# Optimization experiments

Measured on AMD Instinct MI355X. Metric: run time of the kernel, lower is better.

The kernel has to match this reference:

```python
import jax, jax.numpy as jnp
import numpy as np
from jax import lax

NB_ITER = 100
TOL = 1e-6
DN = ('NCHW', 'OIHW', 'NCHW')
PAD = ((1, 1), (1, 1))


def _P(x, kernel):
    # x: [B,H,W] -> [B,3,H,W], conv2d with kernel [3,1,3,3], padding=1
    return lax.conv_general_dilated(x[:, None], kernel, (1, 1), PAD, dimension_numbers=DN)


def _PT(x, kernel):
    # x: [B,3,H,W] -> [B,H,W]; conv_transpose2d(padding=1) == conv2d with
    # spatially-flipped kernel and in/out channels swapped.
    kt = jnp.flip(kernel, (2, 3)).transpose(1, 0, 2, 3)  # [1,3,3,3]
    return lax.conv_general_dilated(x, kt, (1, 1), PAD, dimension_numbers=DN)[:, 0]


def _cg(A, b):
    # Conjugate gradient; original: while i <= 100 and crit >= tol (101 iters max).
    x = b
    r = b - A(x)
    p = r
    crit = jnp.sum(r * r)

    def body(carry, _):
        x, r, p, crit = carry
        active = crit >= TOL
        Ap = A(p)
        denom = jnp.sum(p * Ap)
        alpha = crit / jnp.where(active, denom, 1.0)
        x_n = x + alpha * p
        r_n = r - alpha * Ap
        crit_n = jnp.sum(r_n * r_n)
        beta = crit_n / jnp.where(active, crit, 1.0)
        p_n = r_n + beta * p
        x = jnp.where(active, x_n, x)
        r = jnp.where(active, r_n, r)
        p = jnp.where(active, p_n, p)
        crit = jnp.where(active, crit_n, crit)
        return (x, r, p, crit), None

    (x, _, _, _), _ = lax.scan(body, (x, r, p, crit), None, length=NB_ITER + 1)
    return x


def setup_inputs() -> dict:
    key = jax.random.key(0)
    ks = jax.random.split(key, 6)
    B, C, H, W = 4, 3, 256, 256
    return {
        'mask': jax.random.uniform(ks[0], (B, C, H, W), dtype=jnp.float32),
        'y': jax.random.uniform(ks[1], (B, H, W), dtype=jnp.float32),
        'z': jax.random.normal(ks[2], (B, C, H, W), dtype=jnp.float32),
        'beta': jax.random.normal(ks[3], (B, C, H, W), dtype=jnp.float32),
        'rho': jnp.float32(0.1),
        'kernel': jax.random.uniform(ks[4], (3, 1, 3, 3), dtype=jnp.float32),
    }


def reference(mask, y, z, beta, rho, kernel):
    def A(x):
        # rho*x + adjoint(mask, PT(P(direct(mask, x))))
        d = jnp.sum(mask * x, axis=1)                 # [B,H,W]
        return rho * x + mask * _PT(_P(d, kernel), kernel)[:, None]

    b = mask * _PT(_P(y, kernel), kernel)[:, None] + rho * (z - beta)
    return _cg(A, b)
```

## Files before the change

### kernel.cpp

```cpp
#include <hip/hip_runtime.h>

#define TOL 1e-6f
#define NITER 101
#define H 256
#define W 256
#define HW 65536
#define NBLK 256
#define TPB 256

typedef unsigned long long ull;

#define STRIP_F 768
#define STRIPBUF (NBLK * STRIP_F)
#define WS_CTRL (2 * STRIPBUF)
#define CTRL_F 8192

#define LD_AG(p)    __hip_atomic_load((p), __ATOMIC_RELAXED, __HIP_MEMORY_SCOPE_AGENT)
#define ST_AG(p,v)  __hip_atomic_store((p), (v), __ATOMIC_RELAXED, __HIP_MEMORY_SCOPE_AGENT)

__device__ __forceinline__ unsigned opq0u() {
    unsigned z; asm volatile("s_mov_b32 %0, 0" : "=s"(z)); return z;
}
__device__ __forceinline__ ull opq0ull() {
    return ((ull)opq0u() << 32) | (ull)opq0u();
}
__device__ __forceinline__ float opq0f() { return __uint_as_float(opq0u()); }

__device__ __forceinline__ float frb(float v, unsigned rnd, float* ctrl,
                                     unsigned my_xcc, unsigned xn, unsigned ng) {
    __shared__ float red_[8];
    asm volatile("s_waitcnt vmcnt(0)" ::: "memory");
    #pragma unroll
    for (int off = 32; off; off >>= 1) v += __shfl_down(v, off, 64);
    const int lane = threadIdx.x & 63, wid = threadIdx.x >> 6;
    if (lane == 0) red_[wid] = v;
    __syncthreads();
    if (threadIdx.x == 0) {
        const float part = red_[0] + red_[1] + red_[2] + red_[3];
        float* lval = ctrl + 256 + my_xcc * 256;
        float* gval = ctrl;
        unsigned* cu = (unsigned*)(ctrl + 2304);
        ull* bcast = (ull*)(cu + 320);
        ull* lbc   = (ull*)(cu + 448);
        __hip_atomic_fetch_add(lval + rnd, part, __ATOMIC_RELAXED, __HIP_MEMORY_SCOPE_WORKGROUP);
        asm volatile("s_waitcnt vmcnt(0)" ::: "memory");
        unsigned a = __hip_atomic_fetch_add(cu + my_xcc * 16, 1u,
                         __ATOMIC_RELAXED, __HIP_MEMORY_SCOPE_WORKGROUP);
        ull pk;
        if (a == rnd * xn - 1u) {
            float lsum = __hip_atomic_fetch_add(lval + rnd, opq0f(),
                             __ATOMIC_RELAXED, __HIP_MEMORY_SCOPE_WORKGROUP);
            __hip_atomic_fetch_add(gval + rnd, lsum,
                                   __ATOMIC_RELAXED, __HIP_MEMORY_SCOPE_AGENT);
            asm volatile("s_waitcnt vmcnt(0)" ::: "memory");
            unsigned g = __hip_atomic_fetch_add(cu + 128, 1u,
                             __ATOMIC_RELAXED, __HIP_MEMORY_SCOPE_AGENT);
            if (g == rnd * ng - 1u) {
                float tot = __hip_atomic_fetch_add(gval + rnd, opq0f(),
                                __ATOMIC_RELAXED, __HIP_MEMORY_SCOPE_AGENT);
                pk = ((ull)rnd << 32) | (ull)__float_as_uint(tot);
                #pragma unroll
                for (int xx = 0; xx < 8; ++xx)
                    __hip_atomic_store(bcast + xx * 8, pk,
                                       __ATOMIC_RELAXED, __HIP_MEMORY_SCOPE_AGENT);
            } else {
                for (;;) {
                    pk = __hip_atomic_fetch_add(bcast + my_xcc * 8, opq0ull(),
                             __ATOMIC_RELAXED, __HIP_MEMORY_SCOPE_AGENT);
                    if ((unsigned)(pk >> 32) >= rnd) break;
                    __builtin_amdgcn_s_sleep(2);
                }
            }
            __hip_atomic_store(lbc + my_xcc * 8, pk,
                               __ATOMIC_RELAXED, __HIP_MEMORY_SCOPE_WORKGROUP);
        } else {
            for (;;) {
                pk = __hip_atomic_fetch_add(lbc + my_xcc * 8, opq0ull(),
                         __ATOMIC_RELAXED, __HIP_MEMORY_SCOPE_WORKGROUP);
                if ((unsigned)(pk >> 32) >= rnd) break;
                __builtin_amdgcn_s_sleep(1);
            }
        }
        red_[4] = __uint_as_float((unsigned)(pk & 0xffffffffull));
    }
    __syncthreads();
    return red_[4];
}

__device__ __forceinline__ void ring_pos(int t, int& eh, int& ew) {
    if (t < 72)       { eh = t / 36;                 ew = t - (t / 36) * 36; }
    else if (t < 144) { const int u = t - 72;  eh = 34 + u / 36; ew = u - (u / 36) * 36; }
    else              { const int u = t - 144; eh = 2 + (u >> 2);
                        const int c2 = u & 3;  ew = (c2 < 2) ? c2 : c2 + 32; }
}

__device__ __forceinline__ float4 conv_k2(const float* dext, int row, int wb,
                                          int h0, int w0,
                                          const float* K2sh,
                                          const float* Ctop, const float* Cbot,
                                          const float* CLf, const float* CLt, const float* CLb,
                                          const float* CRf, const float* CRt, const float* CRb)
{
    float q[4] = {0.f, 0.f, 0.f, 0.f};
    float w2s[8], cL[5], cR[5];
    const float* base = dext + row * 36 + wb;
    #pragma unroll
    for (int A = 0; A < 5; ++A) {
        const float4 lo = *(const float4*)(base + A * 36);
        const float4 hi = *(const float4*)(base + A * 36 + 4);
        const float w8[8] = {lo.x, lo.y, lo.z, lo.w, hi.x, hi.y, hi.z, hi.w};
        #pragma unroll
        for (int cc = 0; cc < 4; ++cc) {
            float s = q[cc];
            #pragma unroll
            for (int Bq = 0; Bq < 5; ++Bq)
                s += K2sh[A * 5 + Bq] * w8[cc + Bq];
            q[cc] = s;
        }
        if (A == 2) {
            #pragma unroll
            for (int u = 0; u < 8; ++u) w2s[u] = w8[u];
        }
        cL[A] = w8[2]; cR[A] = w8[5];
    }
    const int gh = h0 + row, gwb = w0 + wb;
    if (gh == 0) {
        #pragma unroll
        for (int cc = 0; cc < 4; ++cc)
            #pragma unroll
            for (int Bq = 0; Bq < 5; ++Bq)
                q[cc] -= Ctop[Bq] * w2s[cc + Bq];
    }
    if (gh == 255) {
        #pragma unroll
        for (int cc = 0; cc < 4; ++cc)
            #pragma unroll
            for (int Bq = 0; Bq < 5; ++Bq)
                q[cc] -= Cbot[Bq] * w2s[cc + Bq];
    }
    if (gwb == 0) {
        const float* C = (gh == 0) ? CLt : ((gh == 255) ? CLb : CLf);
        #pragma unroll
        for (int A = 0; A < 5; ++A) q[0] -= C[A] * cL[A];
    }
    if (gwb == 252) {
        const float* C = (gh == 0) ? CRt : ((gh == 255) ? CRb : CRf);
        #pragma unroll
        for (int A = 0; A < 5; ++A) q[3] -= C[A] * cR[A];
    }
    return make_float4(q[0], q[1], q[2], q[3]);
}

extern "C" __global__ void __launch_bounds__(TPB)
cg_persistent(const float* __restrict__ mask, const float* __restrict__ y,
              const float* __restrict__ z, const float* __restrict__ bet,
              const float* __restrict__ rho_p, const float* __restrict__ kern,
              float* __restrict__ x_out, float* __restrict__ ws)
{
    __shared__ float ksh[27];
    __shared__ __align__(16) float dext[36 * 36];
    __shared__ float m_ring[3][272];
    __shared__ float p_ring[3][272];
    __shared__ float sstage[STRIP_F];
    __shared__ int   ringsrc[272];
    __shared__ float K2sh[25];
    __shared__ float Ctop[5], Cbot[5];
    __shared__ float CLf[5], CLt[5], CLb[5], CRf[5], CRt[5], CRb[5];

    float* strip = ws;
    float* ctrl  = ws + WS_CTRL;

    const int tid = threadIdx.x;
    const int T  = blockIdx.x;
    const int bi = T >> 6;
    const int h0 = ((T >> 3) & 7) << 5;
    const int w0 = (T & 7) << 5;
    const int row = tid >> 3;
    const int wb  = (tid & 7) << 2;
    const int roffb = (h0 + row) * W + (w0 + wb);

    unsigned xcc_raw;
    asm volatile("s_getreg_b32 %0, hwreg(HW_REG_XCC_ID)" : "=s"(xcc_raw));
    const unsigned my_xcc = xcc_raw & 7u;

    unsigned xn = 0, ng = 0;
    unsigned* cu = (unsigned*)(ctrl + 2304);
    if (tid == 0) {
        __hip_atomic_fetch_add(cu + 160 + 16 * my_xcc, 1u,
                               __ATOMIC_RELAXED, __HIP_MEMORY_SCOPE_AGENT);
        __hip_atomic_fetch_add(cu + 144, 1u,
                               __ATOMIC_RELAXED, __HIP_MEMORY_SCOPE_AGENT);
    }

    if (tid < 27) ksh[tid] = kern[tid];
    const float rho = rho_p[0];

    float m_[3][4], x_[3][4], r_[3][4], p_[3][4], Ap_[3][4];
    #pragma unroll
    for (int c = 0; c < 3; ++c) {
        const float4 mv = *(const float4*)(mask + (bi * 3 + c) * HW + roffb);
        m_[c][0] = mv.x; m_[c][1] = mv.y; m_[c][2] = mv.z; m_[c][3] = mv.w;
    }

    for (int t = tid; t < 272; t += TPB) {
        int eh, ew; ring_pos(t, eh, ew);
        const int gh = h0 + eh - 2, gw = w0 + ew - 2;
        const bool valid = (unsigned)gh < (unsigned)H && (unsigned)gw < (unsigned)W;
        int src = -1;
        if (valid) {
            const int tr = gh >> 5, tc = gw >> 5;
            const int Tn = (bi << 6) | (tr << 3) | tc;
            const int lh = gh & 31, lw = gw & 31;
            int idx;
            if (tr != (h0 >> 5)) idx = (lh >= 30) ? 64 + (lh - 30) * 32 + lw : lh * 32 + lw;
            else                 idx = (lw >= 30) ? 192 + lh * 2 + (lw - 30) : 128 + lh * 2 + lw;
            src = Tn * STRIP_F + idx;
        }
        ringsrc[t] = src;
        #pragma unroll
        for (int c = 0; c < 3; ++c) {
            m_ring[c][t] = valid ? mask[(bi * 3 + c) * HW + gh * W + gw] : 0.f;
            p_ring[c][t] = 0.f;
        }
    }

    for (int e = tid; e < 1296; e += TPB) {
        const int eh = e / 36, ew = e - eh * 36;
        const int gh = h0 + eh - 2, gw = w0 + ew - 2;
        dext[e] = ((unsigned)gh < (unsigned)H && (unsigned)gw < (unsigned)W)
                      ? y[bi * HW + gh * W + gw] : 0.f;
    }
    __syncthreads();

    if (tid < 25) {
        const int A = tid / 5, Bq = tid % 5;
        float s = 0.f;
        for (int o = 0; o < 3; ++o)
            for (int i = (A > 2 ? A - 2 : 0); i <= (A < 2 ? A : 2); ++i)
                for (int j = (Bq > 2 ? Bq - 2 : 0); j <= (Bq < 2 ? Bq : 2); ++j)
                    s += ksh[o * 9 + (A - i) * 3 + (Bq - j)] * ksh[o * 9 + (2 - i) * 3 + (2 - j)];
        K2sh[tid] = s;
    } else if (tid < 35) {
        const int Bq = (tid - 25) % 5;
        const int krow = (tid < 30) ? 6 : 0;
        float s = 0.f;
        for (int o = 0; o < 3; ++o)
            for (int j = (Bq > 2 ? Bq - 2 : 0); j <= (Bq < 2 ? Bq : 2); ++j)
                s += ksh[o * 9 + krow + (Bq - j)] * ksh[o * 9 + krow + (2 - j)];
        if (tid < 30) Ctop[Bq] = s; else Cbot[Bq] = s;
    } else if (tid < 65) {
        const int u = tid - 35;
        const int side = u / 15;
        const int v = (u % 15) / 5;
        const int A = u % 5;
        const int kcol = side ? 0 : 2;
        int ilo = (A > 2 ? A - 2 : 0), ihi = (A < 2 ? A : 2);
        if (v == 1 && ilo < 1) ilo = 1;
        if (v == 2 && ihi > 1) ihi = 1;
        float s = 0.f;
        for (int o = 0; o < 3; ++o)
            for (int i = ilo; i <= ihi; ++i)
                s += ksh[o * 9 + (A - i) * 3 + kcol] * ksh[o * 9 + (2 - i) * 3 + kcol];
        float* dst = side ? (v == 0 ? CRf : v == 1 ? CRt : CRb)
                          : (v == 0 ? CLf : v == 1 ? CLt : CLb);
        dst[A] = s;
    }
    __syncthreads();

    {
        const float4 qv = conv_k2(dext, row, wb, h0, w0, K2sh, Ctop, Cbot,
                                  CLf, CLt, CLb, CRf, CRt, CRb);
        const float qa[4] = {qv.x, qv.y, qv.z, qv.w};
        #pragma unroll
        for (int c = 0; c < 3; ++c) {
            const int gi = (bi * 3 + c) * HW + roffb;
            const float4 zv = *(const float4*)(z + gi);
            const float4 bv = *(const float4*)(bet + gi);
            const float zz[4] = {zv.x, zv.y, zv.z, zv.w};
            const float bb[4] = {bv.x, bv.y, bv.z, bv.w};
            #pragma unroll
            for (int cc = 0; cc < 4; ++cc)
                x_[c][cc] = m_[c][cc] * qa[cc] + rho * (zz[cc] - bb[cc]);
        }
    }
    #pragma unroll
    for (int c = 0; c < 3; ++c) {
        if (row < 2) {
            #pragma unroll
            for (int cc = 0; cc < 4; ++cc) sstage[c * 256 + row * 32 + wb + cc] = x_[c][cc];
        }
        if (row >= 30) {
            #pragma unroll
            for (int cc = 0; cc < 4; ++cc) sstage[c * 256 + 64 + (row - 30) * 32 + wb + cc] = x_[c][cc];
        }
        if (wb == 0)  { sstage[c * 256 + 128 + row * 2]     = x_[c][0];
                        sstage[c * 256 + 128 + row * 2 + 1] = x_[c][1]; }
        if (wb == 28) { sstage[c * 256 + 192 + row * 2]     = x_[c][2];
                        sstage[c * 256 + 192 + row * 2 + 1] = x_[c][3]; }
    }
    __syncthreads();
    for (int t = tid; t < STRIP_F; t += TPB)
        ST_AG(strip + T * STRIP_F + t, sstage[t]);

    if (tid == 0) {
        while (__hip_atomic_fetch_add(cu + 144, opq0u(), __ATOMIC_RELAXED,
                                      __HIP_MEMORY_SCOPE_AGENT) < (unsigned)NBLK)
            __builtin_amdgcn_s_sleep(32);
        ng = 0;
        #pragma unroll
        for (int i = 0; i < 8; ++i) {
            unsigned c = __hip_atomic_fetch_add(cu + 160 + 16 * i, opq0u(),
                             __ATOMIC_RELAXED, __HIP_MEMORY_SCOPE_AGENT);
            ng += (c > 0u);
        }
        xn = __hip_atomic_fetch_add(cu + 160 + 16 * my_xcc, opq0u(),
                 __ATOMIC_RELAXED, __HIP_MEMORY_SCOPE_AGENT);
    }
    unsigned rnd = 1;
    frb(0.f, rnd++, ctrl, my_xcc, xn, ng);

    {
        float* dp = dext + (row + 2) * 36 + 2 + wb;
        #pragma unroll
        for (int cc = 0; cc < 4; ++cc)
            dp[cc] = m_[0][cc] * x_[0][cc] + m_[1][cc] * x_[1][cc] + m_[2][cc] * x_[2][cc];
    }
    for (int t = tid; t < 272; t += TPB) {
        int eh, ew; ring_pos(t, eh, ew);
        const int src = ringsrc[t];
        float s = 0.f;
        if (src >= 0) {
            #pragma unroll
            for (int c = 0; c < 3; ++c)
                s += m_ring[c][t] * LD_AG(strip + src + c * 256);
        }
        dext[eh * 36 + ew] = s;
    }
    __syncthreads();
    float csum0 = 0.f;
    {
        const float4 qv = conv_k2(dext, row, wb, h0, w0, K2sh, Ctop, Cbot,
                                  CLf, CLt, CLb, CRf, CRt, CRb);
        const float qa[4] = {qv.x, qv.y, qv.z, qv.w};
        #pragma unroll
        for (int c = 0; c < 3; ++c)
            #pragma unroll
            for (int cc = 0; cc < 4; ++cc) {
                const float b = x_[c][cc];
                const float rv = b - (rho * b + m_[c][cc] * qa[cc]);
                r_[c][cc] = rv; p_[c][cc] = rv;
                csum0 += rv * rv;
            }
    }
    #pragma unroll
    for (int c = 0; c < 3; ++c) {
        if (row < 2) {
            #pragma unroll
            for (int cc = 0; cc < 4; ++cc) sstage[c * 256 + row * 32 + wb + cc] = r_[c][cc];
        }
        if (row >= 30) {
            #pragma unroll
            for (int cc = 0; cc < 4; ++cc) sstage[c * 256 + 64 + (row - 30) * 32 + wb + cc] = r_[c][cc];
        }
        if (wb == 0)  { sstage[c * 256 + 128 + row * 2]     = r_[c][0];
                        sstage[c * 256 + 128 + row * 2 + 1] = r_[c][1]; }
        if (wb == 28) { sstage[c * 256 + 192 + row * 2]     = r_[c][2];
                        sstage[c * 256 + 192 + row * 2 + 1] = r_[c][3]; }
    }
    __syncthreads();
    for (int t = tid; t < STRIP_F; t += TPB)
        ST_AG(strip + STRIPBUF + T * STRIP_F + t, sstage[t]);

    float critj = frb(csum0, rnd++, ctrl, my_xcc, xn, ng);

    for (int t = tid; t < 272; t += TPB) {
        const int src = ringsrc[t];
        if (src >= 0) {
            #pragma unroll
            for (int c = 0; c < 3; ++c)
                p_ring[c][t] = LD_AG(strip + STRIPBUF + src + c * 256);
        }
    }

    for (int j = 0; j < NITER; ++j) {
        const bool active = critj >= TOL;

        {
            float* dp = dext + (row + 2) * 36 + 2 + wb;
            #pragma unroll
            for (int cc = 0; cc < 4; ++cc)
                dp[cc] = m_[0][cc] * p_[0][cc] + m_[1][cc] * p_[1][cc] + m_[2][cc] * p_[2][cc];
        }
        for (int t = tid; t < 272; t += TPB) {
            int eh, ew; ring_pos(t, eh, ew);
            float s = 0.f;
            #pragma unroll
            for (int c = 0; c < 3; ++c) s += m_ring[c][t] * p_ring[c][t];
            dext[eh * 36 + ew] = s;
        }
        __syncthreads();
        float dsum = 0.f;
        {
            const float4 qv = conv_k2(dext, row, wb, h0, w0, K2sh, Ctop, Cbot,
                                      CLf, CLt, CLb, CRf, CRt, CRb);
            const float qa[4] = {qv.x, qv.y, qv.z, qv.w};
            #pragma unroll
            for (int c = 0; c < 3; ++c)
                #pragma unroll
                for (int cc = 0; cc < 4; ++cc) {
                    const float ap = rho * p_[c][cc] + m_[c][cc] * qa[cc];
                    Ap_[c][cc] = ap;
                    dsum += p_[c][cc] * ap;
                }
        }
        const float denom = frb(dsum, rnd++, ctrl, my_xcc, xn, ng);

        const float alpha = critj / (active ? denom : 1.0f);
        float csum = 0.f;
        #pragma unroll
        for (int c = 0; c < 3; ++c)
            #pragma unroll
            for (int cc = 0; cc < 4; ++cc) {
                if (active) {
                    x_[c][cc] += alpha * p_[c][cc];
                    r_[c][cc] -= alpha * Ap_[c][cc];
                }
                csum += r_[c][cc] * r_[c][cc];
            }
        #pragma unroll
        for (int c = 0; c < 3; ++c) {
            if (row < 2) {
                #pragma unroll
                for (int cc = 0; cc < 4; ++cc) sstage[c * 256 + row * 32 + wb + cc] = r_[c][cc];
            }
            if (row >= 30) {
                #pragma unroll
                for (int cc = 0; cc < 4; ++cc) sstage[c * 256 + 64 + (row - 30) * 32 + wb + cc] = r_[c][cc];
            }
            if (wb == 0)  { sstage[c * 256 + 128 + row * 2]     = r_[c][0];
                            sstage[c * 256 + 128 + row * 2 + 1] = r_[c][1]; }
            if (wb == 28) { sstage[c * 256 + 192 + row * 2]     = r_[c][2];
                            sstage[c * 256 + 192 + row * 2 + 1] = r_[c][3]; }
        }
        __syncthreads();
        float* gb = strip + (j & 1) * STRIPBUF;
        for (int t = tid; t < STRIP_F; t += TPB)
            ST_AG(gb + T * STRIP_F + t, sstage[t]);

        const float critn = frb(csum, rnd++, ctrl, my_xcc, xn, ng);

        const float beta = critn / (active ? critj : 1.0f);
        if (active) {
            #pragma unroll
            for (int c = 0; c < 3; ++c)
                #pragma unroll
                for (int cc = 0; cc < 4; ++cc)
                    p_[c][cc] = r_[c][cc] + beta * p_[c][cc];
        }
        for (int t = tid; t < 272; t += TPB) {
            const int src = ringsrc[t];
            if (src >= 0) {
                #pragma unroll
                for (int c = 0; c < 3; ++c) {
                    const float rr = LD_AG(gb + src + c * 256);
                    if (active) p_ring[c][t] = rr + beta * p_ring[c][t];
                }
            }
        }
        critj = critn;
    }

    #pragma unroll
    for (int c = 0; c < 3; ++c)
        *(float4*)(x_out + (bi * 3 + c) * HW + roffb) =
            make_float4(x_[c][0], x_[c][1], x_[c][2], x_[c][3]);
}

extern "C" void kernel_launch(void* const* d_in, const int* in_sizes, int n_in,
                              void* d_out, int out_size, void* d_ws, size_t ws_size,
                              hipStream_t stream)
{
    const float* mask = (const float*)d_in[0];
    const float* y    = (const float*)d_in[1];
    const float* z    = (const float*)d_in[2];
    const float* bet  = (const float*)d_in[3];
    const float* rho  = (const float*)d_in[4];
    const float* kern = (const float*)d_in[5];
    float* x  = (float*)d_out;
    float* ws = (float*)d_ws;

    hipMemsetAsync(ws + WS_CTRL, 0, CTRL_F * sizeof(float), stream);

    void* args[] = { (void*)&mask, (void*)&y, (void*)&z, (void*)&bet,
                     (void*)&rho, (void*)&kern, (void*)&x, (void*)&ws };
    hipLaunchCooperativeKernel((void*)cg_persistent, dim3(NBLK), dim3(TPB),
                               args, 0, stream);
}
```

Measured before the change: 1.314 ms.

## Switch to Chronopoulos-Gear CG with fused dual-value grid reduction

Reformulates the conjugate gradient loop into the single-reduction Chronopoulos-Gear variant. The solver now applies A to r and updates the search direction's image q = Ap by recurrence, so each iteration needs one grid-wide reduction of the pair (r·r, r·Ar) instead of two separate reductions. The global barrier routine is extended to reduce and broadcast two values at once. This halves the cross-XCC synchronisation points per iteration, at the cost of extra halo rings and registers and a small risk of different numerical behaviour and termination near the tolerance.

```diff
diff --git a/kernel.cpp b/kernel.cpp
--- a/kernel.cpp
+++ b/kernel.cpp
@@ -26,65 +26,98 @@
 }
 __device__ __forceinline__ float opq0f() { return __uint_as_float(opq0u()); }
 
-__device__ __forceinline__ float frb(float v, unsigned rnd, float* ctrl,
-                                     unsigned my_xcc, unsigned xn, unsigned ng) {
-    __shared__ float red_[8];
+__device__ __forceinline__ float2 frb2(float va, float vb, unsigned rnd, float* ctrl,
+                                       unsigned my_xcc, unsigned xn, unsigned ng) {
+    __shared__ float redA_[4], redB_[4], out_[2];
     asm volatile("s_waitcnt vmcnt(0)" ::: "memory");
     #pragma unroll
-    for (int off = 32; off; off >>= 1) v += __shfl_down(v, off, 64);
+    for (int off = 32; off; off >>= 1) {
+        va += __shfl_down(va, off, 64);
+        vb += __shfl_down(vb, off, 64);
+    }
     const int lane = threadIdx.x & 63, wid = threadIdx.x >> 6;
-    if (lane == 0) red_[wid] = v;
+    if (lane == 0) { redA_[wid] = va; redB_[wid] = vb; }
     __syncthreads();
     if (threadIdx.x == 0) {
-        const float part = red_[0] + red_[1] + red_[2] + red_[3];
-        float* lval = ctrl + 256 + my_xcc * 256;
-        float* gval = ctrl;
-        unsigned* cu = (unsigned*)(ctrl + 2304);
-        ull* bcast = (ull*)(cu + 320);
-        ull* lbc   = (ull*)(cu + 448);
-        __hip_atomic_fetch_add(lval + rnd, part, __ATOMIC_RELAXED, __HIP_MEMORY_SCOPE_WORKGROUP);
+        const float pa = redA_[0] + redA_[1] + redA_[2] + redA_[3];
+        const float pb = redB_[0] + redB_[1] + redB_[2] + redB_[3];
+        float* gvalA = ctrl;
+        float* gvalB = ctrl + 256;
+        float* lvalA = ctrl + 512  + my_xcc * 256;
+        float* lvalB = ctrl + 2560 + my_xcc * 256;
+        unsigned* cu = (unsigned*)(ctrl + 4608);
+        ull* bcastA = (ull*)(cu + 320);
+        ull* bcastB = (ull*)(cu + 448);
+        ull* lbcA   = (ull*)(cu + 576);
+        ull* lbcB   = (ull*)(cu + 704);
+        __hip_atomic_fetch_add(lvalA + rnd, pa, __ATOMIC_RELAXED, __HIP_MEMORY_SCOPE_WORKGROUP);
+        __hip_atomic_fetch_add(lvalB + rnd, pb, __ATOMIC_RELAXED, __HIP_MEMORY_SCOPE_WORKGROUP);
         asm volatile("s_waitcnt vmcnt(0)" ::: "memory");
         unsigned a = __hip_atomic_fetch_add(cu + my_xcc * 16, 1u,
                          __ATOMIC_RELAXED, __HIP_MEMORY_SCOPE_WORKGROUP);
-        ull pk;
+        ull pkA, pkB;
         if (a == rnd * xn - 1u) {
-            float lsum = __hip_atomic_fetch_add(lval + rnd, opq0f(),
-                             __ATOMIC_RELAXED, __HIP_MEMORY_SCOPE_WORKGROUP);
-            __hip_atomic_fetch_add(gval + rnd, lsum,
-                                   __ATOMIC_RELAXED, __HIP_MEMORY_SCOPE_AGENT);
+            float la = __hip_atomic_fetch_add(lvalA + rnd, opq0f(),
+                           __ATOMIC_RELAXED, __HIP_MEMORY_SCOPE_WORKGROUP);
+            float lb = __hip_atomic_fetch_add(lvalB + rnd, opq0f(),
+                           __ATOMIC_RELAXED, __HIP_MEMORY_SCOPE_WORKGROUP);
+            __hip_atomic_fetch_add(gvalA + rnd, la, __ATOMIC_RELAXED, __HIP_MEMORY_SCOPE_AGENT);
+            __hip_atomic_fetch_add(gvalB + rnd, lb, __ATOMIC_RELAXED, __HIP_MEMORY_SCOPE_AGENT);
             asm volatile("s_waitcnt vmcnt(0)" ::: "memory");
             unsigned g = __hip_atomic_fetch_add(cu + 128, 1u,
                              __ATOMIC_RELAXED, __HIP_MEMORY_SCOPE_AGENT);
             if (g == rnd * ng - 1u) {
-                float tot = __hip_atomic_fetch_add(gval + rnd, opq0f(),
-                                __ATOMIC_RELAXED, __HIP_MEMORY_SCOPE_AGENT);
-                pk = ((ull)rnd << 32) | (ull)__float_as_uint(tot);
+                float ta = __hip_atomic_fetch_add(gvalA + rnd, opq0f(),
+                               __ATOMIC_RELAXED, __HIP_MEMORY_SCOPE_AGENT);
+                float tb = __hip_atomic_fetch_add(gvalB + rnd, opq0f(),
+                               __ATOMIC_RELAXED, __HIP_MEMORY_SCOPE_AGENT);
+                pkA = ((ull)rnd << 32) | (ull)__float_as_uint(ta);
+                pkB = ((ull)rnd << 32) | (ull)__float_as_uint(tb);
                 #pragma unroll
                 for (int xx = 0; xx < 8; ++xx)
-                    __hip_atomic_store(bcast + xx * 8, pk,
+                    __hip_atomic_store(bcastB + xx * 8, pkB,
+                                       __ATOMIC_RELAXED, __HIP_MEMORY_SCOPE_AGENT);
+                #pragma unroll
+                for (int xx = 0; xx < 8; ++xx)
+                    __hip_atomic_store(bcastA + xx * 8, pkA,
                                        __ATOMIC_RELAXED, __HIP_MEMORY_SCOPE_AGENT);
             } else {
                 for (;;) {
-                    pk = __hip_atomic_fetch_add(bcast + my_xcc * 8, opq0ull(),
-                             __ATOMIC_RELAXED, __HIP_MEMORY_SCOPE_AGENT);
-                    if ((unsigned)(pk >> 32) >= rnd) break;
+                    pkA = __hip_atomic_fetch_add(bcastA + my_xcc * 8, opq0ull(),
+                              __ATOMIC_RELAXED, __HIP_MEMORY_SCOPE_AGENT);
+                    if ((unsigned)(pkA >> 32) >= rnd) break;
                     __builtin_amdgcn_s_sleep(2);
                 }
-            }
-            __hip_atomic_store(lbc + my_xcc * 8, pk,
+                for (;;) {
+                    pkB = __hip_atomic_fetch_add(bcastB + my_xcc * 8, opq0ull(),
+                              __ATOMIC_RELAXED, __HIP_MEMORY_SCOPE_AGENT);
+                    if ((unsigned)(pkB >> 32) >= rnd) break;
+                    __builtin_amdgcn_s_sleep(1);
+                }
+            }
+            __hip_atomic_store(lbcB + my_xcc * 8, pkB,
+                               __ATOMIC_RELAXED, __HIP_MEMORY_SCOPE_WORKGROUP);
+            __hip_atomic_store(lbcA + my_xcc * 8, pkA,
                                __ATOMIC_RELAXED, __HIP_MEMORY_SCOPE_WORKGROUP);
         } else {
             for (;;) {
-                pk = __hip_atomic_fetch_add(lbc + my_xcc * 8, opq0ull(),
-                         __ATOMIC_RELAXED, __HIP_MEMORY_SCOPE_WORKGROUP);
-                if ((unsigned)(pk >> 32) >= rnd) break;
+                pkA = __hip_atomic_fetch_add(lbcA + my_xcc * 8, opq0ull(),
+                          __ATOMIC_RELAXED, __HIP_MEMORY_SCOPE_WORKGROUP);
+                if ((unsigned)(pkA >> 32) >= rnd) break;
                 __builtin_amdgcn_s_sleep(1);
             }
-        }
-        red_[4] = __uint_as_float((unsigned)(pk & 0xffffffffull));
-    }
-    __syncthreads();
-    return red_[4];
+            for (;;) {
+                pkB = __hip_atomic_fetch_add(lbcB + my_xcc * 8, opq0ull(),
+                          __ATOMIC_RELAXED, __HIP_MEMORY_SCOPE_WORKGROUP);
+                if ((unsigned)(pkB >> 32) >= rnd) break;
+                __builtin_amdgcn_s_sleep(1);
+            }
+        }
+        out_[0] = __uint_as_float((unsigned)(pkA & 0xffffffffull));
+        out_[1] = __uint_as_float((unsigned)(pkB & 0xffffffffull));
+    }
+    __syncthreads();
+    return make_float2(out_[0], out_[1]);
 }
 
 __device__ __forceinline__ void ring_pos(int t, int& eh, int& ew) {
@@ -160,7 +193,8 @@
     __shared__ float ksh[27];
     __shared__ __align__(16) float dext[36 * 36];
     __shared__ float m_ring[3][272];
-    __shared__ float p_ring[3][272];
+    __shared__ float r_ring[3][272];
+    __shared__ float q_ring[3][272];
     __shared__ float sstage[STRIP_F];
     __shared__ int   ringsrc[272];
     __shared__ float K2sh[25];
@@ -184,7 +218,7 @@
     const unsigned my_xcc = xcc_raw & 7u;
 
     unsigned xn = 0, ng = 0;
-    unsigned* cu = (unsigned*)(ctrl + 2304);
+    unsigned* cu = (unsigned*)(ctrl + 4608);
     if (tid == 0) {
         __hip_atomic_fetch_add(cu + 160 + 16 * my_xcc, 1u,
                                __ATOMIC_RELAXED, __HIP_MEMORY_SCOPE_AGENT);
@@ -195,7 +229,7 @@
     if (tid < 27) ksh[tid] = kern[tid];
     const float rho = rho_p[0];
 
-    float m_[3][4], x_[3][4], r_[3][4], p_[3][4], Ap_[3][4];
+    float m_[3][4], x_[3][4], r_[3][4], p_[3][4], q_[3][4], w_[3][4];
     #pragma unroll
     for (int c = 0; c < 3; ++c) {
         const float4 mv = *(const float4*)(mask + (bi * 3 + c) * HW + roffb);
@@ -220,7 +254,8 @@
         #pragma unroll
         for (int c = 0; c < 3; ++c) {
             m_ring[c][t] = valid ? mask[(bi * 3 + c) * HW + gh * W + gw] : 0.f;
-            p_ring[c][t] = 0.f;
+            r_ring[c][t] = 0.f;
+            q_ring[c][t] = 0.f;
         }
     }
 
@@ -267,6 +302,25 @@
     }
     __syncthreads();
 
+#define STAGE_BORDER(SRC)                                                          \
+    _Pragma("unroll")                                                              \
+    for (int c = 0; c < 3; ++c) {                                                  \
+        if (row < 2) {                                                             \
+            _Pragma("unroll")                                                      \
+            for (int cc = 0; cc < 4; ++cc)                                         \
+                sstage[c * 256 + row * 32 + wb + cc] = SRC[c][cc];                 \
+        }                                                                          \
+        if (row >= 30) {                                                           \
+            _Pragma("unroll")                                                      \
+            for (int cc = 0; cc < 4; ++cc)                                         \
+                sstage[c * 256 + 64 + (row - 30) * 32 + wb + cc] = SRC[c][cc];     \
+        }                                                                          \
+        if (wb == 0)  { sstage[c * 256 + 128 + row * 2]     = SRC[c][0];           \
+                        sstage[c * 256 + 128 + row * 2 + 1] = SRC[c][1]; }         \
+        if (wb == 28) { sstage[c * 256 + 192 + row * 2]     = SRC[c][2];           \
+                        sstage[c * 256 + 192 + row * 2 + 1] = SRC[c][3]; }         \
+    }
+
     {
         const float4 qv = conv_k2(dext, row, wb, h0, w0, K2sh, Ctop, Cbot,
                                   CLf, CLt, CLb, CRf, CRt, CRb);
@@ -283,21 +337,7 @@
                 x_[c][cc] = m_[c][cc] * qa[cc] + rho * (zz[cc] - bb[cc]);
         }
     }
-    #pragma unroll
-    for (int c = 0; c < 3; ++c) {
-        if (row < 2) {
-            #pragma unroll
-            for (int cc = 0; cc < 4; ++cc) sstage[c * 256 + row * 32 + wb + cc] = x_[c][cc];
-        }
-        if (row >= 30) {
-            #pragma unroll
-            for (int cc = 0; cc < 4; ++cc) sstage[c * 256 + 64 + (row - 30) * 32 + wb + cc] = x_[c][cc];
-        }
-        if (wb == 0)  { sstage[c * 256 + 128 + row * 2]     = x_[c][0];
-                        sstage[c * 256 + 128 + row * 2 + 1] = x_[c][1]; }
-        if (wb == 28) { sstage[c * 256 + 192 + row * 2]     = x_[c][2];
-                        sstage[c * 256 + 192 + row * 2 + 1] = x_[c][3]; }
-    }
+    STAGE_BORDER(x_)
     __syncthreads();
     for (int t = tid; t < STRIP_F; t += TPB)
         ST_AG(strip + T * STRIP_F + t, sstage[t]);
@@ -317,7 +357,7 @@
                  __ATOMIC_RELAXED, __HIP_MEMORY_SCOPE_AGENT);
     }
     unsigned rnd = 1;
-    frb(0.f, rnd++, ctrl, my_xcc, xn, ng);
+    frb2(0.f, 0.f, rnd++, ctrl, my_xcc, xn, ng);
 
     {
         float* dp = dext + (row + 2) * 36 + 2 + wb;
@@ -337,7 +377,7 @@
         dext[eh * 36 + ew] = s;
     }
     __syncthreads();
-    float csum0 = 0.f;
+    float gsum0 = 0.f;
     {
         const float4 qv = conv_k2(dext, row, wb, h0, w0, K2sh, Ctop, Cbot,
                                   CLf, CLt, CLb, CRf, CRt, CRb);
@@ -349,57 +389,103 @@
                 const float b = x_[c][cc];
                 const float rv = b - (rho * b + m_[c][cc] * qa[cc]);
                 r_[c][cc] = rv; p_[c][cc] = rv;
-                csum0 += rv * rv;
-            }
-    }
-    #pragma unroll
-    for (int c = 0; c < 3; ++c) {
-        if (row < 2) {
-            #pragma unroll
-            for (int cc = 0; cc < 4; ++cc) sstage[c * 256 + row * 32 + wb + cc] = r_[c][cc];
-        }
-        if (row >= 30) {
-            #pragma unroll
-            for (int cc = 0; cc < 4; ++cc) sstage[c * 256 + 64 + (row - 30) * 32 + wb + cc] = r_[c][cc];
-        }
-        if (wb == 0)  { sstage[c * 256 + 128 + row * 2]     = r_[c][0];
-                        sstage[c * 256 + 128 + row * 2 + 1] = r_[c][1]; }
-        if (wb == 28) { sstage[c * 256 + 192 + row * 2]     = r_[c][2];
-                        sstage[c * 256 + 192 + row * 2 + 1] = r_[c][3]; }
-    }
+                gsum0 += rv * rv;
+            }
+    }
+    STAGE_BORDER(r_)
     __syncthreads();
     for (int t = tid; t < STRIP_F; t += TPB)
         ST_AG(strip + STRIPBUF + T * STRIP_F + t, sstage[t]);
 
-    float critj = frb(csum0, rnd++, ctrl, my_xcc, xn, ng);
+    float gamma = frb2(gsum0, 0.f, rnd++, ctrl, my_xcc, xn, ng).x;
 
     for (int t = tid; t < 272; t += TPB) {
         const int src = ringsrc[t];
         if (src >= 0) {
             #pragma unroll
             for (int c = 0; c < 3; ++c)
-                p_ring[c][t] = LD_AG(strip + STRIPBUF + src + c * 256);
-        }
-    }
+                r_ring[c][t] = LD_AG(strip + STRIPBUF + src + c * 256);
+        }
+    }
+
+    {
+        float* dp = dext + (row + 2) * 36 + 2 + wb;
+        #pragma unroll
+        for (int cc = 0; cc < 4; ++cc)
+            dp[cc] = m_[0][cc] * r_[0][cc] + m_[1][cc] * r_[1][cc] + m_[2][cc] * r_[2][cc];
+    }
+    for (int t = tid; t < 272; t += TPB) {
+        int eh, ew; ring_pos(t, eh, ew);
+        float s = 0.f;
+        #pragma unroll
+        for (int c = 0; c < 3; ++c) s += m_ring[c][t] * r_ring[c][t];
+        dext[eh * 36 + ew] = s;
+    }
+    __syncthreads();
+    float dsum0 = 0.f;
+    {
+        const float4 qv = conv_k2(dext, row, wb, h0, w0, K2sh, Ctop, Cbot,
+                                  CLf, CLt, CLb, CRf, CRt, CRb);
+        const float qa[4] = {qv.x, qv.y, qv.z, qv.w};
+        #pragma unroll
+        for (int c = 0; c < 3; ++c)
+            #pragma unroll
+            for (int cc = 0; cc < 4; ++cc) {
+                const float wv = rho * r_[c][cc] + m_[c][cc] * qa[cc];
+                q_[c][cc] = wv;
+                dsum0 += r_[c][cc] * wv;
+            }
+    }
+    STAGE_BORDER(q_)
+    __syncthreads();
+    for (int t = tid; t < STRIP_F; t += TPB)
+        ST_AG(strip + T * STRIP_F + t, sstage[t]);
+
+    const float delta0 = frb2(dsum0, 0.f, rnd++, ctrl, my_xcc, xn, ng).x;
+
+    for (int t = tid; t < 272; t += TPB) {
+        const int src = ringsrc[t];
+        if (src >= 0) {
+            #pragma unroll
+            for (int c = 0; c < 3; ++c)
+                q_ring[c][t] = LD_AG(strip + src + c * 256);
+        }
+    }
+    float alpha = (gamma >= TOL) ? (gamma / delta0) : 0.f;
 
     for (int j = 0; j < NITER; ++j) {
-        const bool active = critj >= TOL;
+        const bool active = (gamma >= TOL);
+
+        if (active) {
+            #pragma unroll
+            for (int c = 0; c < 3; ++c)
+                #pragma unroll
+                for (int cc = 0; cc < 4; ++cc) {
+                    x_[c][cc] += alpha * p_[c][cc];
+                    r_[c][cc] -= alpha * q_[c][cc];
+                }
+            for (int t = tid; t < 272; t += TPB) {
+                #pragma unroll
+                for (int c = 0; c < 3; ++c)
+                    r_ring[c][t] -= alpha * q_ring[c][t];
+            }
+        }
 
         {
             float* dp = dext + (row + 2) * 36 + 2 + wb;
             #pragma unroll
             for (int cc = 0; cc < 4; ++cc)
-                dp[cc] = m_[0][cc] * p_[0][cc] + m_[1][cc] * p_[1][cc] + m_[2][cc] * p_[2][cc];
+                dp[cc] = m_[0][cc] * r_[0][cc] + m_[1][cc] * r_[1][cc] + m_[2][cc] * r_[2][cc];
         }
         for (int t = tid; t < 272; t += TPB) {
             int eh, ew; ring_pos(t, eh, ew);
             float s = 0.f;
             #pragma unroll
-            for (int c = 0; c < 3; ++c) s += m_ring[c][t] * p_ring[c][t];
+            for (int c = 0; c < 3; ++c) s += m_ring[c][t] * r_ring[c][t];
             dext[eh * 36 + ew] = s;
         }
         __syncthreads();
-        float dsum = 0.f;
+        float gsum = 0.f, dsum = 0.f;
         {
             const float4 qv = conv_k2(dext, row, wb, h0, w0, K2sh, Ctop, Cbot,
                                       CLf, CLt, CLb, CRf, CRt, CRb);
@@ -408,66 +494,45 @@
             for (int c = 0; c < 3; ++c)
                 #pragma unroll
                 for (int cc = 0; cc < 4; ++cc) {
-                    const float ap = rho * p_[c][cc] + m_[c][cc] * qa[cc];
-                    Ap_[c][cc] = ap;
-                    dsum += p_[c][cc] * ap;
+                    const float rv = r_[c][cc];
+                    const float wv = rho * rv + m_[c][cc] * qa[cc];
+                    w_[c][cc] = wv;
+                    gsum += rv * rv;
+                    dsum += rv * wv;
                 }
         }
-        const float denom = frb(dsum, rnd++, ctrl, my_xcc, xn, ng);
-
-        const float alpha = critj / (active ? denom : 1.0f);
-        float csum = 0.f;
-        #pragma unroll
-        for (int c = 0; c < 3; ++c)
-            #pragma unroll
-            for (int cc = 0; cc < 4; ++cc) {
-                if (active) {
-                    x_[c][cc] += alpha * p_[c][cc];
-                    r_[c][cc] -= alpha * Ap_[c][cc];
-                }
-                csum += r_[c][cc] * r_[c][cc];
-            }
-        #pragma unroll
-        for (int c = 0; c < 3; ++c) {
-            if (row < 2) {
-                #pragma unroll
-                for (int cc = 0; cc < 4; ++cc) sstage[c * 256 + row * 32 + wb + cc] = r_[c][cc];
-            }
-            if (row >= 30) {
-                #pragma unroll
-                for (int cc = 0; cc < 4; ++cc) sstage[c * 256 + 64 + (row - 30) * 32 + wb + cc] = r_[c][cc];
-            }
-            if (wb == 0)  { sstage[c * 256 + 128 + row * 2]     = r_[c][0];
-                            sstage[c * 256 + 128 + row * 2 + 1] = r_[c][1]; }
-            if (wb == 28) { sstage[c * 256 + 192 + row * 2]     = r_[c][2];
-                            sstage[c * 256 + 192 + row * 2 + 1] = r_[c][3]; }
-        }
+        STAGE_BORDER(w_)
         __syncthreads();
-        float* gb = strip + (j & 1) * STRIPBUF;
+        float* gb = strip + ((j + 1) & 1) * STRIPBUF;
         for (int t = tid; t < STRIP_F; t += TPB)
             ST_AG(gb + T * STRIP_F + t, sstage[t]);
 
-        const float critn = frb(csum, rnd++, ctrl, my_xcc, xn, ng);
-
-        const float beta = critn / (active ? critj : 1.0f);
+        const float2 gd = frb2(gsum, dsum, rnd++, ctrl, my_xcc, xn, ng);
+
         if (active) {
+            const float gp = gd.x, dp = gd.y;
+            const float beta = gp / gamma;
+            const float alphan = gp / (dp - beta * gp / alpha);
             #pragma unroll
             for (int c = 0; c < 3; ++c)
                 #pragma unroll
-                for (int cc = 0; cc < 4; ++cc)
+                for (int cc = 0; cc < 4; ++cc) {
                     p_[c][cc] = r_[c][cc] + beta * p_[c][cc];
-        }
-        for (int t = tid; t < 272; t += TPB) {
-            const int src = ringsrc[t];
-            if (src >= 0) {
-                #pragma unroll
-                for (int c = 0; c < 3; ++c) {
-                    const float rr = LD_AG(gb + src + c * 256);
-                    if (active) p_ring[c][t] = rr + beta * p_ring[c][t];
+                    q_[c][cc] = w_[c][cc] + beta * q_[c][cc];
                 }
-            }
-        }
-        critj = critn;
+            for (int t = tid; t < 272; t += TPB) {
+                const int src = ringsrc[t];
+                if (src >= 0) {
+                    #pragma unroll
+                    for (int c = 0; c < 3; ++c) {
+                        const float wn = LD_AG(gb + src + c * 256);
+                        q_ring[c][t] = wn + beta * q_ring[c][t];
+                    }
+                }
+            }
+            gamma = gp;
+            alpha = alphan;
+        }
     }
 
     #pragma unroll
```

New measurement: 1.100 ms. 16.2% less time.
